# Optimization experiments

Measured on AMD Instinct MI355X. Metric: run time of the kernel, lower is better.

Reference implementation:

```python
import jax, jax.numpy as jnp
import numpy as np

# M = batch16 * (128^2+64^2+32^2+16^2+8^2) FPN pixels for 1024x1024 inputs, strides 8..128
M = 349184
C = 80          # num_classes
N_POS = 2048    # positive center locations

ALPHA = 0.25        # hm_focal_alpha
BETA = 4.0          # hm_focal_beta
GAMMA = 2.0         # loss_gamma
SIGMOID_CLAMP = 1e-4
POS_W = 1.0
NEG_W = 1.0
REG_W = 2.0         # reg_weight


def setup_inputs() -> dict:
    key = jax.random.key(0)
    k1, k2, k3, k4, k5, k6 = jax.random.split(key, 6)
    return {
        'logits_pred': jax.random.normal(k1, (M, C), jnp.float32),
        'flattened_hms': jax.random.uniform(k2, (M, C), jnp.float32),
        'reg_pred': jax.random.uniform(k3, (M, 4), jnp.float32),
        'reg_targets': jax.random.normal(k4, (M, 4), jnp.float32),
        'pos_inds': jax.random.randint(k5, (N_POS,), 0, M),
        'labels': jax.random.randint(k6, (N_POS,), 0, C),
    }


def _giou_loss(pred, target):
    # pred/target: [M,4] ltrb distances from grid point to box edges
    pl, pt, pr, pb = pred[:, 0], pred[:, 1], pred[:, 2], pred[:, 3]
    tl, tt, tr, tb = target[:, 0], target[:, 1], target[:, 2], target[:, 3]
    target_area = (tl + tr) * (tt + tb)
    pred_area = (pl + pr) * (pt + pb)
    w_intersect = jnp.minimum(pl, tl) + jnp.minimum(pr, tr)
    h_intersect = jnp.minimum(pb, tb) + jnp.minimum(pt, tt)
    g_w = jnp.maximum(pl, tl) + jnp.maximum(pr, tr)
    g_h = jnp.maximum(pb, tb) + jnp.maximum(pt, tt)
    ac_union = g_w * g_h
    area_intersect = w_intersect * h_intersect
    area_union = target_area + pred_area - area_intersect
    ious = (area_intersect + 1.0) / (area_union + 1.0)
    gious = ious - (ac_union - area_union) / (ac_union + 1e-7)
    return 1.0 - gious  # per-pixel giou loss


def reference(logits_pred, flattened_hms, reg_pred, reg_targets, pos_inds, labels):
    # ---- heatmap focal loss (CenterNet2 heatmap_focal_loss) ----
    pred = jnp.clip(jax.nn.sigmoid(logits_pred), SIGMOID_CLAMP, 1.0 - SIGMOID_CLAMP)
    neg_weights = (1.0 - flattened_hms) ** BETA  # zero at exact positives
    pos_pred = pred[pos_inds, labels]            # irregular gather, [N]
    pos_loss = jnp.log(pos_pred) * (1.0 - pos_pred) ** GAMMA
    neg_loss = jnp.log(1.0 - pred) * pred ** GAMMA * neg_weights
    pos_loss = -ALPHA * jnp.sum(pos_loss)
    neg_loss = -(1.0 - ALPHA) * jnp.sum(neg_loss)
    num_pos_avg = float(max(N_POS, 1))
    pos_loss = POS_W * pos_loss / num_pos_avg
    neg_loss = NEG_W * neg_loss / num_pos_avg

    valid = jnp.max(reg_targets, axis=1) >= 0  # [M] bool, replaces nonzero-gather
    # not_norm_reg=True -> per-location weight 1 on valid rows
    w = valid.astype(reg_pred.dtype)
    safe_targets = jnp.where(valid[:, None], reg_targets, 1.0)
    per_px = _giou_loss(reg_pred, safe_targets)
    reg_norm = jnp.maximum(jnp.sum(w), 1.0)
    reg_loss = REG_W * jnp.sum(per_px * w) / reg_norm

    return jnp.stack([pos_loss, neg_loss, reg_loss])
```

## Files before the change

### kernel.cpp

```cpp
#include <hip/hip_runtime.h>
#include <math.h>

#define M_ROWS   349184
#define C_CH     80
#define NPOS     2048
#define ALPHA    0.25f
#define SIG_CLMP 1.0e-4f
#define REG_W    2.0f

#define NBLOCKS  2048
#define NTHREADS 256
#define N4       6983680
#define CHUNK    3410

__device__ __forceinline__ float fast_rcp(float x) {
    return __builtin_amdgcn_rcpf(x);
}

__device__ __forceinline__ float clamped_sigmoid(float x) {
    float e = __expf(-x);
    float p = fast_rcp(1.0f + e);
    return fminf(fmaxf(p, SIG_CLMP), 1.0f - SIG_CLMP);
}

__device__ __forceinline__ float neg_term(float x, float h) {
    float p = clamped_sigmoid(x);
    float q = 1.0f - h;
    float q2 = q * q;
    return __logf(1.0f - p) * (p * p) * (q2 * q2);
}

__device__ __forceinline__ float neg_term4(float4 x, float4 h) {
    return neg_term(x.x, h.x) + neg_term(x.y, h.y) +
           neg_term(x.z, h.z) + neg_term(x.w, h.w);
}

__global__ __launch_bounds__(NTHREADS) void centernet_loss_main(
    const float* __restrict__ logits,
    const float* __restrict__ hms,
    const float* __restrict__ reg_pred,
    const float* __restrict__ reg_tgt,
    const int*   __restrict__ pos_inds,
    const int*   __restrict__ labels,
    float4* __restrict__ partials)
{
    const int t   = threadIdx.x;
    const int tid = blockIdx.x * NTHREADS + t;

    float neg = 0.0f, giou = 0.0f, wsum = 0.0f, pos = 0.0f;

    const float4* lg4 = (const float4*)logits;
    const float4* hm4 = (const float4*)hms;

    const int start = blockIdx.x * CHUNK;
    const int end   = start + CHUNK;

    int i = start + t;
    for (; i + 3 * NTHREADS < end; i += 4 * NTHREADS) {
        float4 x0 = lg4[i];
        float4 x1 = lg4[i + NTHREADS];
        float4 x2 = lg4[i + 2 * NTHREADS];
        float4 x3 = lg4[i + 3 * NTHREADS];
        float4 h0 = hm4[i];
        float4 h1 = hm4[i + NTHREADS];
        float4 h2 = hm4[i + 2 * NTHREADS];
        float4 h3 = hm4[i + 3 * NTHREADS];
        neg += neg_term4(x0, h0);
        neg += neg_term4(x1, h1);
        neg += neg_term4(x2, h2);
        neg += neg_term4(x3, h3);
    }
    for (; i < end; i += NTHREADS) {
        neg += neg_term4(lg4[i], hm4[i]);
    }

    const int rstart = blockIdx.x * 171;
    const int rend   = min(rstart + 171, M_ROWS);
    const float4* rp4 = (const float4*)reg_pred;
    const float4* rt4 = (const float4*)reg_tgt;
    for (int r = rstart + t; r < rend; r += NTHREADS) {
        float4 tt = rt4[r];
        float mx = fmaxf(fmaxf(tt.x, tt.y), fmaxf(tt.z, tt.w));
        if (mx >= 0.0f) {
            float4 p = rp4[r];
            float target_area = (tt.x + tt.z) * (tt.y + tt.w);
            float pred_area   = (p.x + p.z) * (p.y + p.w);
            float w_int = fminf(p.x, tt.x) + fminf(p.z, tt.z);
            float h_int = fminf(p.w, tt.w) + fminf(p.y, tt.y);
            float g_w   = fmaxf(p.x, tt.x) + fmaxf(p.z, tt.z);
            float g_h   = fmaxf(p.w, tt.w) + fmaxf(p.y, tt.y);
            float ac    = g_w * g_h;
            float ai    = w_int * h_int;
            float au    = target_area + pred_area - ai;
            float ious  = (ai + 1.0f) * fast_rcp(au + 1.0f);
            float gious = ious - (ac - au) * fast_rcp(ac + 1e-7f);
            giou += 1.0f - gious;
            wsum += 1.0f;
        }
    }

    if (t == 0 && blockIdx.x < NPOS) {
        int k = blockIdx.x;
        int idx = pos_inds[k] * C_CH + labels[k];
        float p  = clamped_sigmoid(logits[idx]);
        float om = 1.0f - p;
        pos = __logf(p) * om * om;
    }

    const int lane = t & 63;
    const int wave = t >> 6;
    #pragma unroll
    for (int off = 32; off > 0; off >>= 1) {
        neg  += __shfl_down(neg,  off);
        giou += __shfl_down(giou, off);
        wsum += __shfl_down(wsum, off);
        pos  += __shfl_down(pos,  off);
    }
    __shared__ float smem[4][4];
    if (lane == 0) {
        smem[wave][0] = neg;  smem[wave][1] = giou;
        smem[wave][2] = wsum; smem[wave][3] = pos;
    }
    __syncthreads();
    if (t == 0) {
        float4 v;
        v.x = smem[0][0] + smem[1][0] + smem[2][0] + smem[3][0];
        v.y = smem[0][1] + smem[1][1] + smem[2][1] + smem[3][1];
        v.z = smem[0][2] + smem[1][2] + smem[2][2] + smem[3][2];
        v.w = smem[0][3] + smem[1][3] + smem[2][3] + smem[3][3];
        partials[blockIdx.x] = v;
    }
}

__global__ __launch_bounds__(256) void centernet_loss_reduce(
    const float4* __restrict__ partials,
    float* __restrict__ out)
{
    float neg = 0.0f, giou = 0.0f, wsum = 0.0f, pos = 0.0f;
    for (int i = threadIdx.x; i < NBLOCKS; i += 256) {
        float4 v = partials[i];
        neg += v.x; giou += v.y; wsum += v.z; pos += v.w;
    }
    const int lane = threadIdx.x & 63;
    const int wave = threadIdx.x >> 6;
    #pragma unroll
    for (int off = 32; off > 0; off >>= 1) {
        neg  += __shfl_down(neg,  off);
        giou += __shfl_down(giou, off);
        wsum += __shfl_down(wsum, off);
        pos  += __shfl_down(pos,  off);
    }
    __shared__ float smem[4][4];
    if (lane == 0) {
        smem[wave][0] = neg;  smem[wave][1] = giou;
        smem[wave][2] = wsum; smem[wave][3] = pos;
    }
    __syncthreads();
    if (threadIdx.x == 0) {
        float n = smem[0][0] + smem[1][0] + smem[2][0] + smem[3][0];
        float g = smem[0][1] + smem[1][1] + smem[2][1] + smem[3][1];
        float w = smem[0][2] + smem[1][2] + smem[2][2] + smem[3][2];
        float p = smem[0][3] + smem[1][3] + smem[2][3] + smem[3][3];
        const float inv_npos = 1.0f / (float)NPOS;
        out[0] = -ALPHA * p * inv_npos;
        out[1] = -(1.0f - ALPHA) * n * inv_npos;
        out[2] = REG_W * g / fmaxf(w, 1.0f);
    }
}

extern "C" void kernel_launch(void* const* d_in, const int* in_sizes, int n_in,
                              void* d_out, int out_size, void* d_ws, size_t ws_size,
                              hipStream_t stream) {
    const float* logits   = (const float*)d_in[0];
    const float* hms      = (const float*)d_in[1];
    const float* reg_pred = (const float*)d_in[2];
    const float* reg_tgt  = (const float*)d_in[3];
    const int*   pos_inds = (const int*)d_in[4];
    const int*   labels   = (const int*)d_in[5];
    float* out = (float*)d_out;
    float4* partials = (float4*)d_ws;

    centernet_loss_main<<<NBLOCKS, NTHREADS, 0, stream>>>(
        logits, hms, reg_pred, reg_tgt, pos_inds, labels, partials);
    centernet_loss_reduce<<<1, 256, 0, stream>>>(partials, out);
}
```

Baseline: 256.4 us.

## Use 512 blocks of 1024 threads with nontemporal loads and swizzled block mapping

Reorganizes the main kernel from 2048 blocks of 256 threads into 512 blocks of 1024 threads, each handling four times as much heatmap data, regression rows and positive gathers. The streaming logits and heatmap reads now use nontemporal loads to avoid polluting the cache. Block indices are remapped by interleaving so adjacent launched blocks touch non-adjacent chunks. The goal is less per-block overhead and better bandwidth, at the cost of lower occupancy flexibility and a 16-wave shared-memory reduction.

```diff
diff --git a/kernel.cpp b/kernel.cpp
--- a/kernel.cpp
+++ b/kernel.cpp
@@ -8,18 +8,21 @@
 #define SIG_CLMP 1.0e-4f
 #define REG_W    2.0f
 
-#define NBLOCKS  2048
-#define NTHREADS 256
+#define NBLOCKS  512
+#define NTHREADS 1024
 #define N4       6983680
-#define CHUNK    3410
+#define CHUNK4   13640
+#define ROWS_PB  682
+#define POS_PB   4
+
+typedef float vf4 __attribute__((ext_vector_type(4)));
 
 __device__ __forceinline__ float fast_rcp(float x) {
     return __builtin_amdgcn_rcpf(x);
 }
 
 __device__ __forceinline__ float clamped_sigmoid(float x) {
-    float e = __expf(-x);
-    float p = fast_rcp(1.0f + e);
+    float p = fast_rcp(1.0f + __expf(-x));
     return fminf(fmaxf(p, SIG_CLMP), 1.0f - SIG_CLMP);
 }
 
@@ -30,9 +33,13 @@
     return __logf(1.0f - p) * (p * p) * (q2 * q2);
 }
 
-__device__ __forceinline__ float neg_term4(float4 x, float4 h) {
+__device__ __forceinline__ float neg_term4(vf4 x, vf4 h) {
     return neg_term(x.x, h.x) + neg_term(x.y, h.y) +
            neg_term(x.z, h.z) + neg_term(x.w, h.w);
+}
+
+__device__ __forceinline__ vf4 ldnt4(const vf4* p) {
+    return __builtin_nontemporal_load(p);
 }
 
 __global__ __launch_bounds__(NTHREADS) void centernet_loss_main(
@@ -44,45 +51,44 @@
     const int*   __restrict__ labels,
     float4* __restrict__ partials)
 {
-    const int t   = threadIdx.x;
-    const int tid = blockIdx.x * NTHREADS + t;
+    const int t = threadIdx.x;
+    const int b = ((int)blockIdx.x & 255) * 2 + ((int)blockIdx.x >> 8);
 
     float neg = 0.0f, giou = 0.0f, wsum = 0.0f, pos = 0.0f;
 
-    const float4* lg4 = (const float4*)logits;
-    const float4* hm4 = (const float4*)hms;
+    const vf4* lg4 = (const vf4*)logits;
+    const vf4* hm4 = (const vf4*)hms;
 
-    const int start = blockIdx.x * CHUNK;
-    const int end   = start + CHUNK;
+    const int start = b * CHUNK4;
+    const int end   = start + CHUNK4;
 
     int i = start + t;
     for (; i + 3 * NTHREADS < end; i += 4 * NTHREADS) {
-        float4 x0 = lg4[i];
-        float4 x1 = lg4[i + NTHREADS];
-        float4 x2 = lg4[i + 2 * NTHREADS];
-        float4 x3 = lg4[i + 3 * NTHREADS];
-        float4 h0 = hm4[i];
-        float4 h1 = hm4[i + NTHREADS];
-        float4 h2 = hm4[i + 2 * NTHREADS];
-        float4 h3 = hm4[i + 3 * NTHREADS];
+        vf4 x0 = ldnt4(&lg4[i]);
+        vf4 x1 = ldnt4(&lg4[i + NTHREADS]);
+        vf4 x2 = ldnt4(&lg4[i + 2 * NTHREADS]);
+        vf4 x3 = ldnt4(&lg4[i + 3 * NTHREADS]);
+        vf4 h0 = ldnt4(&hm4[i]);
+        vf4 h1 = ldnt4(&hm4[i + NTHREADS]);
+        vf4 h2 = ldnt4(&hm4[i + 2 * NTHREADS]);
+        vf4 h3 = ldnt4(&hm4[i + 3 * NTHREADS]);
         neg += neg_term4(x0, h0);
         neg += neg_term4(x1, h1);
         neg += neg_term4(x2, h2);
         neg += neg_term4(x3, h3);
     }
     for (; i < end; i += NTHREADS) {
-        neg += neg_term4(lg4[i], hm4[i]);
+        neg += neg_term4(ldnt4(&lg4[i]), ldnt4(&hm4[i]));
     }
 
-    const int rstart = blockIdx.x * 171;
-    const int rend   = min(rstart + 171, M_ROWS);
-    const float4* rp4 = (const float4*)reg_pred;
-    const float4* rt4 = (const float4*)reg_tgt;
-    for (int r = rstart + t; r < rend; r += NTHREADS) {
-        float4 tt = rt4[r];
+    const int rstart = b * ROWS_PB;
+    const vf4* rp4 = (const vf4*)reg_pred;
+    const vf4* rt4 = (const vf4*)reg_tgt;
+    for (int r = rstart + t; r < rstart + ROWS_PB; r += NTHREADS) {
+        vf4 tt = rt4[r];
         float mx = fmaxf(fmaxf(tt.x, tt.y), fmaxf(tt.z, tt.w));
         if (mx >= 0.0f) {
-            float4 p = rp4[r];
+            vf4 p = rp4[r];
             float target_area = (tt.x + tt.z) * (tt.y + tt.w);
             float pred_area   = (p.x + p.z) * (p.y + p.w);
             float w_int = fminf(p.x, tt.x) + fminf(p.z, tt.z);
@@ -99,8 +105,8 @@
         }
     }
 
-    if (t == 0 && blockIdx.x < NPOS) {
-        int k = blockIdx.x;
+    if (t < POS_PB) {
+        int k = b * POS_PB + t;
         int idx = pos_inds[k] * C_CH + labels[k];
         float p  = clamped_sigmoid(logits[idx]);
         float om = 1.0f - p;
@@ -116,18 +122,19 @@
         wsum += __shfl_down(wsum, off);
         pos  += __shfl_down(pos,  off);
     }
-    __shared__ float smem[4][4];
+    __shared__ float smem[16][4];
     if (lane == 0) {
         smem[wave][0] = neg;  smem[wave][1] = giou;
         smem[wave][2] = wsum; smem[wave][3] = pos;
     }
     __syncthreads();
     if (t == 0) {
-        float4 v;
-        v.x = smem[0][0] + smem[1][0] + smem[2][0] + smem[3][0];
-        v.y = smem[0][1] + smem[1][1] + smem[2][1] + smem[3][1];
-        v.z = smem[0][2] + smem[1][2] + smem[2][2] + smem[3][2];
-        v.w = smem[0][3] + smem[1][3] + smem[2][3] + smem[3][3];
+        float4 v = make_float4(0.f, 0.f, 0.f, 0.f);
+        #pragma unroll
+        for (int w = 0; w < 16; ++w) {
+            v.x += smem[w][0]; v.y += smem[w][1];
+            v.z += smem[w][2]; v.w += smem[w][3];
+        }
         partials[blockIdx.x] = v;
     }
 }
```

Result: faster. 234.5 us (-8.6%).
